# Performance work log

Measured on AMD Instinct MI355X. Metric: run time of the kernel, lower is better.

## Reference

```python
import jax, jax.numpy as jnp
import numpy as np

B = 2048
REAL_NL = 500
NL = 504            # ceil(500/8)*8
NZ = 50
NC = 21
GH = 512            # gru hidden
LRF = 336           # low_res_features
CHS = [336, 168, 84, 42]  # deconv channel ladder
EPS = 1e-5


def setup_inputs() -> dict:
    key = jax.random.key(0)
    ks = iter(jax.random.split(key, 40))
    d = {}
    d["X"] = jax.random.normal(next(ks), (B, REAL_NL, NC), dtype=jnp.float32)
    d["z"] = jax.random.normal(next(ks), (B, NZ), dtype=jnp.float32)
    d["is_training"] = 0
    # Upsampler dense: Linear(NZ -> NL//8 * LRF)
    d["dense_W"] = jax.random.normal(next(ks), (NL // 8 * LRF, NZ), dtype=jnp.float32) * 0.05
    d["dense_b"] = jnp.zeros((NL // 8 * LRF,), dtype=jnp.float32)
    for i in range(3):
        cin, cout = CHS[i], CHS[i + 1]
        d[f"dc{i}_W"] = jax.random.normal(next(ks), (cin, cout, 2), dtype=jnp.float32) * 0.05
        d[f"bn{i}_g"] = jnp.ones((cout,), dtype=jnp.float32)
        d[f"bn{i}_b"] = jnp.zeros((cout,), dtype=jnp.float32)
        d[f"bn{i}_m"] = jax.random.normal(next(ks), (cout,), dtype=jnp.float32) * 0.1
        d[f"bn{i}_v"] = jax.random.uniform(next(ks), (cout,), dtype=jnp.float32, minval=0.5, maxval=1.5)
        d[f"prelu{i}"] = jnp.full((1,), 0.25, dtype=jnp.float32)
    # project_x: Conv1d(NC->NC, k=1) == linear
    d["w_px"] = jax.random.normal(next(ks), (NC, NC), dtype=jnp.float32) * 0.05
    d["b_px"] = jnp.zeros((NC,), dtype=jnp.float32)
    # GRU (1 layer): input = 42 + NC = 63
    gin = CHS[3] + NC
    d["w_ih"] = jax.random.normal(next(ks), (3 * GH, gin), dtype=jnp.float32) * 0.05
    d["w_hh"] = jax.random.normal(next(ks), (3 * GH, GH), dtype=jnp.float32) * 0.05
    d["b_ih"] = jnp.zeros((3 * GH,), dtype=jnp.float32)
    d["b_hh"] = jnp.zeros((3 * GH,), dtype=jnp.float32)
    # output_x: Conv1d(GH->NC, k=1)
    d["w_out"] = jax.random.normal(next(ks), (NC, GH), dtype=jnp.float32) * 0.05
    d["b_out"] = jnp.zeros((NC,), dtype=jnp.float32)
    return d


def _upsample(z, dense_W, dense_b, dcs, bns, alphas):
    b = z.shape[0]
    h = (z @ dense_W.T + dense_b).reshape(b, LRF, NL // 8)  # [B, 336, 63]
    for i in range(3):
        W = dcs[i]  # [cin, cout, 2]
        t = h.shape[-1]
        # ConvTranspose1d k=2 s=2: out[..., 2t+k] = sum_c in[...,c,t] * W[c,:,k]
        h = jnp.einsum('bct,cok->botk', h, W).reshape(b, W.shape[1], 2 * t)
        g, bb, m, v = bns[i]
        h = (h - m[:, None]) * (g[:, None] / jnp.sqrt(v[:, None] + EPS)) + bb[:, None]
        a = alphas[i]
        h = jnp.where(h >= 0, h, a[0] * h)
    return h  # [B, 42, NL]


def reference(X, z, is_training,
              dense_W, dense_b,
              dc0_W, bn0_g, bn0_b, bn0_m, bn0_v, prelu0,
              dc1_W, bn1_g, bn1_b, bn1_m, bn1_v, prelu1,
              dc2_W, bn2_g, bn2_b, bn2_m, bn2_v, prelu2,
              w_px, b_px, w_ih, w_hh, b_ih, b_hh, w_out, b_out):
    h = _upsample(z, dense_W, dense_b,
                  [dc0_W, dc1_W, dc2_W],
                  [(bn0_g, bn0_b, bn0_m, bn0_v), (bn1_g, bn1_b, bn1_m, bn1_v), (bn2_g, bn2_b, bn2_m, bn2_v)],
                  [prelu0, prelu1, prelu2])
    b = z.shape[0]
    hseq = jnp.transpose(h, (2, 0, 1))  # [NL, B, 42]

    def step(carry, h_t):
        gru_h, x1h = carry                       # [B,GH], [B,NC]
        px = x1h @ w_px.T + b_px                 # project_x (1x1 conv)
        x_in = jnp.concatenate([h_t, px], axis=-1)  # [B, 63]
        gi = x_in @ w_ih.T + b_ih
        gh = gru_h @ w_hh.T + b_hh
        ir, iz, inn = jnp.split(gi, 3, axis=-1)
        hr, hz, hn = jnp.split(gh, 3, axis=-1)
        r = jax.nn.sigmoid(ir + hr)
        zt = jax.nn.sigmoid(iz + hz)
        n = jnp.tanh(inn + r * hn)
        h_new = (1.0 - zt) * n + zt * gru_h
        logit = h_new @ w_out.T + b_out          # [B, NC]
        x1h_new = jax.nn.one_hot(jnp.argmax(logit, axis=-1), NC, dtype=logit.dtype)
        return (h_new, x1h_new), logit

    init = (jnp.zeros((b, GH), dtype=z.dtype), jnp.zeros((b, NC), dtype=z.dtype))
    _, logits = jax.lax.scan(step, init, hseq)   # [NL, B, NC]
    out = jnp.transpose(logits, (1, 0, 2))[:, :REAL_NL, :]
    return out
```

## Files before the change

### kernel.cpp

```cpp
#include <hip/hip_runtime.h>
#include <math.h>

#define NLFULL 504
#define REAL_NL 500
#define BATCH 2048
#define NZ 50
#define NC 21
#define GHID 512
#define EPSB 1e-5f
#define LO_SCALE 2048.0f
#define INV_LO (1.0f / 2048.0f)

typedef __attribute__((ext_vector_type(4))) float f32x4;
typedef __attribute__((ext_vector_type(8))) _Float16 half8;

__device__ __forceinline__ void split2(float x, _Float16& hi, _Float16& lo) {
    hi = (_Float16)x;
    lo = (_Float16)((x - (float)hi) * LO_SCALE);
}

__global__ __launch_bounds__(512) void upsample_kernel(
    const float* __restrict__ z, const float* __restrict__ dW, const float* __restrict__ db,
    const float* __restrict__ W0, const float* __restrict__ g0, const float* __restrict__ bb0,
    const float* __restrict__ m0, const float* __restrict__ v0, const float* __restrict__ al0,
    const float* __restrict__ W1, const float* __restrict__ g1, const float* __restrict__ bb1,
    const float* __restrict__ m1, const float* __restrict__ v1, const float* __restrict__ al1,
    const float* __restrict__ W2, const float* __restrict__ g2, const float* __restrict__ bb2,
    const float* __restrict__ m2, const float* __restrict__ v2, const float* __restrict__ al2,
    float* __restrict__ hseq)
{
    __shared__ float bufA[5712];
    __shared__ float bufB[5544];
    __shared__ float zl[52];

    const int b   = blockIdx.x;
    const int ta  = blockIdx.y * 16;
    const int nt0 = min(16, 63 - ta);
    const int tid = threadIdx.x;

    if (tid < NZ) zl[tid] = z[b * NZ + tid];
    __syncthreads();

    for (int i = tid; i < 336 * nt0; i += 512) {
        int c = i % 336, tt = i / 336;
        int row = c * 63 + ta + tt;
        const float* wr = dW + (size_t)row * NZ;
        float s = db[row];
        #pragma unroll
        for (int n = 0; n < NZ; ++n) s += zl[n] * wr[n];
        bufA[c * 17 + tt] = s;
    }
    __syncthreads();

    const float a0 = al0[0], a1 = al1[0], a2 = al2[0];

    for (int i = tid; i < 168 * 2 * nt0; i += 512) {
        int o = i % 168, tt1 = i / 168;
        int tt = tt1 >> 1, k = tt1 & 1;
        const float* wp = W0 + o * 2 + k;
        float s = 0.f;
        for (int c = 0; c < 336; ++c) s += bufA[c * 17 + tt] * wp[c * 336];
        float sc = g0[o] / sqrtf(v0[o] + EPSB);
        s = (s - m0[o]) * sc + bb0[o];
        s = (s >= 0.f) ? s : a0 * s;
        bufB[o * 33 + tt1] = s;
    }
    __syncthreads();

    for (int i = tid; i < 84 * 4 * nt0; i += 512) {
        int o = i % 84, tt2 = i / 84;
        int tt1 = tt2 >> 1, k = tt2 & 1;
// ... 27 lines not shown
{
    int i = blockIdx.x * 256 + threadIdx.x;
    if (i >= 22 * 1536) return;
    int e = i / 1536, jg = i % 1536;
    const float* wih = w_ih + jg * 63 + 42;
    float s = b_ih[jg];
    #pragma unroll
    for (int jp = 0; jp < NC; ++jp) {
        float px = b_px[jp] + (e < NC ? w_px[jp * NC + e] : 0.f);
        s += px * wih[jp];
    }
    table[i] = s;
}

__global__ void pack_whh_kernel(const float* __restrict__ w_hh,
                                _Float16* __restrict__ pH, _Float16* __restrict__ pL)
{
    int i = blockIdx.x * 256 + threadIdx.x;
    if (i >= 3 * 32 * 16 * 512) return;
    int e = i & 7, l = (i >> 3) & 63, kf = (i >> 9) & 15, nf = (i >> 13) & 31, g = i >> 18;
    int n = nf * 16 + (l & 15);
    int k = kf * 32 + ((l >> 4) << 3) + e;
    float v = w_hh[(size_t)(g * GHID + n) * GHID + k];
    _Float16 hi, lo; split2(v, hi, lo);
    pH[i] = hi; pL[i] = lo;
}

__global__ void pack_wih_kernel(const float* __restrict__ w_ih,
                                _Float16* __restrict__ pH, _Float16* __restrict__ pL)
{
    int i = blockIdx.x * 256 + threadIdx.x;
    if (i >= 3 * 32 * 2 * 512) return;
    int e = i & 7, l = (i >> 3) & 63, kf = (i >> 9) & 1, nf = (i >> 10) & 31, g = i >> 15;
    int n = nf * 16 + (l & 15);
    int k = kf * 32 + ((l >> 4) << 3) + e;
    float v = (k < 42) ? w_ih[(size_t)(g * GHID + n) * 63 + k] : 0.f;
    _Float16 hi, lo; split2(v, hi, lo);
    pH[i] = hi; pL[i] = lo;
}

__global__ void pack_wout_kernel(const float* __restrict__ w_out,
                                 _Float16* __restrict__ pH, _Float16* __restrict__ pL)
{
    int i = blockIdx.x * 256 + threadIdx.x;
    if (i >= 2 * 16 * 512) return;
    int e = i & 7, l = (i >> 3) & 63, kf = (i >> 9) & 15, nf = i >> 13;
    int n = nf * 16 + (l & 15);
    int k = kf * 32 + ((l >> 4) << 3) + e;
    float v = (n < NC) ? w_out[(size_t)n * GHID + k] : 0.f;
    _Float16 hi, lo; split2(v, hi, lo);
    pH[i] = hi; pL[i] = lo;
}

__global__ void init_kernel(_Float16* __restrict__ hH, _Float16* __restrict__ hL)
{
    int i = blockIdx.x * 256 + threadIdx.x;
    if (i < BATCH * GHID) { hH[i] = (_Float16)0.f; hL[i] = (_Float16)0.f; }
}

#define MFMA3(mainA, crossA, aH_, aL_, bH_, bL_)                                   \
    mainA  = __builtin_amdgcn_mfma_f32_16x16x32_f16(aH_, bH_, mainA, 0, 0, 0);     \
    crossA = __builtin_amdgcn_mfma_f32_16x16x32_f16(aH_, bL_, crossA, 0, 0, 0);    \
    crossA = __builtin_amdgcn_mfma_f32_16x16x32_f16(aL_, bH_, crossA, 0, 0, 0);

__global__ __launch_bounds__(512, 2) void gru_step(
    const _Float16* __restrict__ hpH, const _Float16* __restrict__ hpL,
    const float* __restrict__ ht,
    const float* __restrict__ table,
    const _Float16* __restrict__ whhH, const _Float16* __restrict__ whhL,
    const _Float16* __restrict__ wihH, const _Float16* __restrict__ wihL,
    const float* __restrict__ b_hh,
    const _Float16* __restrict__ woH, const _Float16* __restrict__ woL,
    const float* __restrict__ b_out,
    float* __restrict__ out, int t,
    _Float16* __restrict__ hnH, _Float16* __restrict__ hnL)
{
    __shared__ float lg[128][33];
    __shared__ int   idx_lds[128];

    const int tid  = threadIdx.x;
    const int l    = tid & 63;
    const int wv   = tid >> 6;
    const int m0   = blockIdx.y * 128;
    const int lrow = l & 15;
    const int lk   = (l >> 4) << 3;

    if (t > 0) {
        const size_t ar = (size_t)(m0 + wv * 16 + lrow) * GHID + lk;
        f32x4 accM[2], accX[2];
        accM[0] = (f32x4)0.f; accM[1] = (f32x4)0.f;
        accX[0] = (f32x4)0.f; accX[1] = (f32x4)0.f;
        for (int kf = 0; kf < 16; ++kf) {
            half8 aH = *(const half8*)(hpH + ar + kf * 32);
            half8 aL = *(const half8*)(hpL + ar + kf * 32);
            #pragma unroll
            for (int nf = 0; nf < 2; ++nf) {
                size_t bo = ((size_t)(nf * 16 + kf) << 9) + (l << 3);
                half8 bH = *(const half8*)(woH + bo);
                half8 bL = *(const half8*)(woL + bo);
                MFMA3(accM[nf], accX[nf], aH, aL, bH, bL);
            }
        }
        #pragma unroll
        for (int nf = 0; nf < 2; ++nf) {
            int col = nf * 16 + lrow;
            float bias = (col < NC) ? b_out[col] : 0.f;
            #pragma unroll
            for (int r = 0; r < 4; ++r) {
                int row = wv * 16 + ((l >> 4) << 2) + r;
                lg[row][col] = accM[nf][r] + accX[nf][r] * INV_LO + bias;
            }
        }
    }
    __syncthreads();
    if (tid < 128) {
        if (t > 0) {
            float best = lg[tid][0]; int bi = 0;
            #pragma unroll
            for (int c = 1; c < NC; ++c) {
                float v = lg[tid][c];
                if (v > best) { best = v; bi = c; }
            }
            idx_lds[tid] = bi;
            if (blockIdx.x == 0) {
                float* op = out + (size_t)(m0 + tid) * (REAL_NL * NC) + (size_t)(t - 1) * NC;
                #pragma unroll
                for (int c = 0; c < NC; ++c) op[c] = lg[tid][c];
            }
        } else {
            idx_lds[tid] = NC;
        }
    }
    __syncthreads();

    if (t >= REAL_NL) return;

    const int wM = wv >> 1, wN = wv & 1;
    const int mw = m0 + wM * 32;
    const int nf = blockIdx.x * 2 + wN;

    f32x4 aM[4][2], aX[4][2];
    #pragma unroll
    for (int s = 0; s < 4; ++s)
        #pragma unroll
        for (int mi = 0; mi < 2; ++mi) { aM[s][mi] = (f32x4)0.f; aX[s][mi] = (f32x4)0.f; }

    const size_t arow0 = (size_t)(mw + lrow) * GHID + lk;
    const size_t arow1 = arow0 + 16 * GHID;

    for (int kf = 0; kf < 16; ++kf) {
        half8 aHf[2], aLf[2];
        aHf[0] = *(const half8*)(hpH + arow0 + kf * 32);
        aLf[0] = *(const half8*)(hpL + arow0 + kf * 32);
        aHf[1] = *(const half8*)(hpH + arow1 + kf * 32);
        aLf[1] = *(const half8*)(hpL + arow1 + kf * 32);
        #pragma unroll
        for (int g = 0; g < 3; ++g) {
            size_t bo = ((size_t)((g * 32 + nf) * 16 + kf) << 9) + (l << 3);
            half8 bH = *(const half8*)(whhH + bo);
            half8 bL = *(const half8*)(whhL + bo);
            const int s = (g == 2) ? 3 : g;
            #pragma unroll
            for (int mi = 0; mi < 2; ++mi) {
                MFMA3(aM[s][mi], aX[s][mi], aHf[mi], aLf[mi], bH, bL);
            }
        }
    }

    #pragma unroll
    for (int kf = 0; kf < 2; ++kf) {
        half8 aHf[2], aLf[2];
        #pragma unroll
        for (int mi = 0; mi < 2; ++mi) {
            const float* rp = ht + (size_t)(mw + mi * 16 + lrow) * 42;
            #pragma unroll
            for (int e = 0; e < 8; ++e) {
                int k = kf * 32 + lk + e;
                float f = (k < 42) ? rp[k] : 0.f;
                _Float16 hi, lo; split2(f, hi, lo);
                aHf[mi][e] = hi; aLf[mi][e] = lo;
            }
        }
        #pragma unroll
        for (int g = 0; g < 3; ++g) {
            size_t bo = ((size_t)((g * 32 + nf) * 2 + kf) << 9) + (l << 3);
            half8 bH = *(const half8*)(wihH + bo);
            half8 bL = *(const half8*)(wihL + bo);
            const int s = (g == 2) ? 2 : g;
            #pragma unroll
            for (int mi = 0; mi < 2; ++mi) {
                MFMA3(aM[s][mi], aX[s][mi], aHf[mi], aLf[mi], bH, bL);
            }
        }
    }

    const int c = nf * 16 + lrow;
    const float bhr = b_hh[c], bhz = b_hh[GHID + c], bhn = b_hh[2 * GHID + c];
    #pragma unroll
    for (int mi = 0; mi < 2; ++mi) {
        #pragma unroll
        for (int r = 0; r < 4; ++r) {
            int lm = wM * 32 + mi * 16 + ((l >> 4) << 2) + r;
            int m = m0 + lm;
            const float* tb = table + idx_lds[lm] * 1536;
            float rv  = aM[0][mi][r] + aX[0][mi][r] * INV_LO + bhr + tb[c];
            float zv  = aM[1][mi][r] + aX[1][mi][r] * INV_LO + bhz + tb[GHID + c];
            float inp = aM[2][mi][r] + aX[2][mi][r] * INV_LO + tb[2 * GHID + c];
            float hnp = aM[3][mi][r] + aX[3][mi][r] * INV_LO + bhn;
            float rg = 1.f / (1.f + expf(-rv));
            float zg = 1.f / (1.f + expf(-zv));
            float ng = tanhf(inp + rg * hnp);
            size_t off = (size_t)m * GHID + c;
            float hpv = (float)hpH[off] + (float)hpL[off] * INV_LO;
            float hnv = (1.f - zg) * ng + zg * hpv;
            _Float16 hi, lo; split2(hnv, hi, lo);
            hnH[off] = hi; hnL[off] = lo;
        }
    }
}

extern "C" void kernel_launch(void* const* d_in, const int* in_sizes, int n_in,
                              void* d_out, int out_size, void* d_ws, size_t ws_size,
                              hipStream_t stream)
{
    const float* z    = (const float*)d_in[1];
    const float* dW   = (const float*)d_in[3];
    const float* db   = (const float*)d_in[4];
    const float* W0   = (const float*)d_in[5];
    const float* g0   = (const float*)d_in[6];
    const float* bb0  = (const float*)d_in[7];
    const float* m0   = (const float*)d_in[8];
    const float* v0   = (const float*)d_in[9];
    const float* al0  = (const float*)d_in[10];
    const float* W1   = (const float*)d_in[11];
    const float* g1   = (const float*)d_in[12];
    const float* bb1  = (const float*)d_in[13];
    const float* m1   = (const float*)d_in[14];
    const float* v1   = (const float*)d_in[15];
    const float* al1  = (const float*)d_in[16];
    const float* W2   = (const float*)d_in[17];
    const float* g2   = (const float*)d_in[18];
    const float* bb2  = (const float*)d_in[19];
    const float* m2   = (const float*)d_in[20];
    const float* v2   = (const float*)d_in[21];
    const float* al2  = (const float*)d_in[22];
    const float* w_px = (const float*)d_in[23];
    const float* b_px = (const float*)d_in[24];
    const float* w_ih = (const float*)d_in[25];
    const float* w_hh = (const float*)d_in[26];
    const float* b_ih = (const float*)d_in[27];
    const float* b_hh = (const float*)d_in[28];
    const float* w_out= (const float*)d_in[29];
    const float* b_out= (const float*)d_in[30];
    float* out = (float*)d_out;

    float* ws = (float*)d_ws;
    float* hseq = ws;
    _Float16* hAH = (_Float16*)(hseq + (size_t)NLFULL * BATCH * 42);
    _Float16* hAL = hAH + (size_t)BATCH * GHID;
    _Float16* hBH = hAL + (size_t)BATCH * GHID;
    _Float16* hBL = hBH + (size_t)BATCH * GHID;
    _Float16* whhH = hBL + (size_t)BATCH * GHID;
    _Float16* whhL = whhH + 3 * 32 * 16 * 512;
    _Float16* wihH = whhL + 3 * 32 * 16 * 512;
    _Float16* wihL = wihH + 3 * 32 * 2 * 512;
    _Float16* woH  = wihL + 3 * 32 * 2 * 512;
    _Float16* woL  = woH + 2 * 16 * 512;
    float* table = (float*)(woL + 2 * 16 * 512);

    upsample_kernel<<<dim3(BATCH, 4), 512, 0, stream>>>(
        z, dW, db,
        W0, g0, bb0, m0, v0, al0,
        W1, g1, bb1, m1, v1, al1,
        W2, g2, bb2, m2, v2, al2,
        hseq);

    table_kernel<<<(22 * 1536 + 255) / 256, 256, 0, stream>>>(w_px, b_px, w_ih, b_ih, table);
    pack_whh_kernel<<<(3 * 32 * 16 * 512 + 255) / 256, 256, 0, stream>>>(w_hh, whhH, whhL);
    pack_wih_kernel<<<(3 * 32 * 2 * 512 + 255) / 256, 256, 0, stream>>>(w_ih, wihH, wihL);
    pack_wout_kernel<<<(2 * 16 * 512 + 255) / 256, 256, 0, stream>>>(w_out, woH, woL);
    init_kernel<<<(BATCH * GHID + 255) / 256, 256, 0, stream>>>(hAH, hAL);

    for (int t = 0; t <= REAL_NL; ++t) {
        const _Float16* pH = (t & 1) ? hBH : hAH;
        const _Float16* pL = (t & 1) ? hBL : hAL;
        _Float16* nH = (t & 1) ? hAH : hBH;
        _Float16* nL = (t & 1) ? hAL : hBL;
        gru_step<<<dim3(16, 16), 512, 0, stream>>>(
            pH, pL, hseq + (size_t)t * BATCH * 42, table,
            whhH, whhL, wihH, wihL, b_hh,
            woH, woL, b_out, out, t, nH, nL);
    }
}
```

Baseline: 34.50 ms.

## Replace per-timestep GRU launches with persistent cooperative kernel and grid barrier

Replaces 501 separate gru_step launches with one persistent cooperative kernel of 256 blocks. The blocks synchronize each timestep through an atomic counter barrier in global memory. The hidden state is stored as interleaved hi/lo fp16 pairs packed into one 32-bit word and read and written with agent-scope relaxed atomics. The tiling also changes to 64-row by 128-column blocks, and the output projection is fused into the same pass over h as the recurrent GEMM. This removes launch overhead and per-step kernel boundaries. The costs are spin-barrier latency, possible visibility or ordering problems from relaxed atomics, and a deadlock risk if the fallback launch does not make all blocks co-resident.

```diff
diff --git a/kernel.cpp b/kernel.cpp
--- a/kernel.cpp
+++ b/kernel.cpp
@@ -13,10 +13,45 @@
 
 typedef __attribute__((ext_vector_type(4))) float f32x4;
 typedef __attribute__((ext_vector_type(8))) _Float16 half8;
+typedef __attribute__((ext_vector_type(4))) unsigned uint4v;
 
 __device__ __forceinline__ void split2(float x, _Float16& hi, _Float16& lo) {
     hi = (_Float16)x;
     lo = (_Float16)((x - (float)hi) * LO_SCALE);
+}
+__device__ __forceinline__ unsigned packh(float x) {
+    _Float16 hi, lo; split2(x, hi, lo);
+    return (unsigned)__builtin_bit_cast(unsigned short, hi)
+         | ((unsigned)__builtin_bit_cast(unsigned short, lo) << 16);
+}
+__device__ __forceinline__ float unpackh(unsigned w) {
+    _Float16 hi = __builtin_bit_cast(_Float16, (unsigned short)(w & 0xFFFFu));
+    _Float16 lo = __builtin_bit_cast(_Float16, (unsigned short)(w >> 16));
+    return (float)hi + (float)lo * INV_LO;
+}
+
+__device__ __forceinline__ void load_hfrag(const unsigned* H, size_t eoff,
+                                           half8& aH, half8& aL) {
+    unsigned long long* p = (unsigned long long*)(H + eoff);
+    unsigned long long d0 = __hip_atomic_load(p + 0, __ATOMIC_RELAXED, __HIP_MEMORY_SCOPE_AGENT);
+    unsigned long long d1 = __hip_atomic_load(p + 1, __ATOMIC_RELAXED, __HIP_MEMORY_SCOPE_AGENT);
+    unsigned long long d2 = __hip_atomic_load(p + 2, __ATOMIC_RELAXED, __HIP_MEMORY_SCOPE_AGENT);
+    unsigned long long d3 = __hip_atomic_load(p + 3, __ATOMIC_RELAXED, __HIP_MEMORY_SCOPE_AGENT);
+    unsigned w0 = (unsigned)d0, w1 = (unsigned)(d0 >> 32);
+    unsigned w2 = (unsigned)d1, w3 = (unsigned)(d1 >> 32);
+    unsigned w4 = (unsigned)d2, w5 = (unsigned)(d2 >> 32);
+    unsigned w6 = (unsigned)d3, w7 = (unsigned)(d3 >> 32);
+    uint4v hw, lw;
+    hw.x = (w0 & 0xFFFFu) | (w1 << 16);
+    hw.y = (w2 & 0xFFFFu) | (w3 << 16);
+    hw.z = (w4 & 0xFFFFu) | (w5 << 16);
+    hw.w = (w6 & 0xFFFFu) | (w7 << 16);
+    lw.x = (w0 >> 16) | (w1 & 0xFFFF0000u);
+    lw.y = (w2 >> 16) | (w3 & 0xFFFF0000u);
+    lw.z = (w4 >> 16) | (w5 & 0xFFFF0000u);
+    lw.w = (w6 >> 16) | (w7 & 0xFFFF0000u);
+    aH = __builtin_bit_cast(half8, hw);
+    aL = __builtin_bit_cast(half8, lw);
 }
 
 __global__ __launch_bounds__(512) void upsample_kernel(
@@ -150,10 +185,11 @@
     pH[i] = hi; pL[i] = lo;
 }
 
-__global__ void init_kernel(_Float16* __restrict__ hH, _Float16* __restrict__ hL)
+__global__ void init_kernel(unsigned* __restrict__ hA, int* __restrict__ bar)
 {
     int i = blockIdx.x * 256 + threadIdx.x;
-    if (i < BATCH * GHID) { hH[i] = (_Float16)0.f; hL[i] = (_Float16)0.f; }
+    if (i < BATCH * GHID) hA[i] = 0u;
+    if (i < 64) bar[i] = 0;
 }
 
 #define MFMA3(mainA, crossA, aH_, aL_, bH_, bL_)                                   \
@@ -161,158 +197,163 @@
     crossA = __builtin_amdgcn_mfma_f32_16x16x32_f16(aH_, bL_, crossA, 0, 0, 0);    \
     crossA = __builtin_amdgcn_mfma_f32_16x16x32_f16(aL_, bH_, crossA, 0, 0, 0);
 
-__global__ __launch_bounds__(512, 2) void gru_step(
-    const _Float16* __restrict__ hpH, const _Float16* __restrict__ hpL,
-    const float* __restrict__ ht,
-    const float* __restrict__ table,
-    const _Float16* __restrict__ whhH, const _Float16* __restrict__ whhL,
-    const _Float16* __restrict__ wihH, const _Float16* __restrict__ wihL,
-    const float* __restrict__ b_hh,
-    const _Float16* __restrict__ woH, const _Float16* __restrict__ woL,
-    const float* __restrict__ b_out,
-    float* __restrict__ out, int t,
-    _Float16* __restrict__ hnH, _Float16* __restrict__ hnL)
-{
-    __shared__ float lg[128][33];
-    __shared__ int   idx_lds[128];
-
-    const int tid  = threadIdx.x;
-    const int l    = tid & 63;
-    const int wv   = tid >> 6;
-    const int m0   = blockIdx.y * 128;
-    const int lrow = l & 15;
-    const int lk   = (l >> 4) << 3;
-
-    if (t > 0) {
-        const size_t ar = (size_t)(m0 + wv * 16 + lrow) * GHID + lk;
-        f32x4 accM[2], accX[2];
-        accM[0] = (f32x4)0.f; accM[1] = (f32x4)0.f;
-        accX[0] = (f32x4)0.f; accX[1] = (f32x4)0.f;
+struct GruP {
+    unsigned *hA, *hB;
+    const float* hseq;
+    const float* table;
+    const _Float16 *whhH, *whhL, *wihH, *wihL, *woH, *woL;
+    const float *b_hh, *b_out;
+    float* out;
+    int* bar;
+};
+
+__global__ __launch_bounds__(512, 1) void gru_persistent(GruP p)
+{
+    __shared__ float lgbuf[64][33];
+    __shared__ int   idx_l[64];
+
+    const int bid = blockIdx.x;
+    const int nb  = bid & 7;
+    const int mb  = bid >> 3;
+    const int m0  = mb * 64;
+    const int tid = threadIdx.x;
+    const int l   = tid & 63, wv = tid >> 6;
+    const int mw  = wv >> 1, nw = wv & 1;
+    const int lrow = l & 15, lk = (l >> 4) << 3;
+
+    const int rowg = m0 + mw * 16 + lrow;
+    const size_t abase = (size_t)rowg * GHID;
+    const int nf0 = nb * 4 + nw * 2;
+    int epoch = 0;
+
+    for (int i = 1; i <= REAL_NL + 1; ++i) {
+        __syncthreads();
+        ++epoch;
+        if (tid == 0) {
+            __hip_atomic_fetch_add(p.bar, 1, __ATOMIC_RELEASE, __HIP_MEMORY_SCOPE_AGENT);
+            while (__hip_atomic_load(p.bar, __ATOMIC_RELAXED, __HIP_MEMORY_SCOPE_AGENT)
+                   < epoch * 256)
+                __builtin_amdgcn_s_sleep(1);
+        }
+        __syncthreads();
+
+        const unsigned* Hp = (i & 1) ? p.hA : p.hB;
+        unsigned*       Hn = (i & 1) ? p.hB : p.hA;
+        const float*    ht = p.hseq + (size_t)(i - 1) * (BATCH * 42);
+        const bool    do_g = (i <= REAL_NL);
+
+        f32x4 gM[4][2], gX[4][2];
+        f32x4 lM = (f32x4)0.f, lX = (f32x4)0.f;
+        #pragma unroll
+        for (int s = 0; s < 4; ++s)
+            #pragma unroll
+            for (int cc = 0; cc < 2; ++cc) { gM[s][cc] = (f32x4)0.f; gX[s][cc] = (f32x4)0.f; }
+
         for (int kf = 0; kf < 16; ++kf) {
-            half8 aH = *(const half8*)(hpH + ar + kf * 32);
-            half8 aL = *(const half8*)(hpL + ar + kf * 32);
+            half8 aH, aL;
+            load_hfrag(Hp, abase + kf * 32 + lk, aH, aL);
+            {
+                size_t bo = ((size_t)(nw * 16 + kf) << 9) + (l << 3);
+                half8 bH = *(const half8*)(p.woH + bo);
+                half8 bL = *(const half8*)(p.woL + bo);
+                MFMA3(lM, lX, aH, aL, bH, bL);
+            }
+            if (do_g) {
+                #pragma unroll
+                for (int g = 0; g < 3; ++g) {
+                    #pragma unroll
+                    for (int cc = 0; cc < 2; ++cc) {
+                        size_t bo = ((size_t)((g * 32 + nf0 + cc) * 16 + kf) << 9) + (l << 3);
+                        half8 bH = *(const half8*)(p.whhH + bo);
+                        half8 bL = *(const half8*)(p.whhL + bo);
+                        const int s = (g == 2) ? 3 : g;
+                        MFMA3(gM[s][cc], gX[s][cc], aH, aL, bH, bL);
+                    }
+                }
+            }
+        }
+
+        if (do_g) {
             #pragma unroll
-            for (int nf = 0; nf < 2; ++nf) {
-                size_t bo = ((size_t)(nf * 16 + kf) << 9) + (l << 3);
-                half8 bH = *(const half8*)(woH + bo);
-                half8 bL = *(const half8*)(woL + bo);
-                MFMA3(accM[nf], accX[nf], aH, aL, bH, bL);
-            }
-        }
-        #pragma unroll
-        for (int nf = 0; nf < 2; ++nf) {
-            int col = nf * 16 + lrow;
-            float bias = (col < NC) ? b_out[col] : 0.f;
+            for (int kf = 0; kf < 2; ++kf) {
+                half8 aH, aL;
+                const float* rp = ht + (size_t)rowg * 42;
+                #pragma unroll
+                for (int e = 0; e < 8; ++e) {
+                    int k = kf * 32 + lk + e;
+                    float f = (k < 42) ? rp[k] : 0.f;
+                    _Float16 hi, lo; split2(f, hi, lo);
+                    aH[e] = hi; aL[e] = lo;
+                }
+                #pragma unroll
+                for (int g = 0; g < 3; ++g) {
+                    #pragma unroll
+                    for (int cc = 0; cc < 2; ++cc) {
+                        size_t bo = ((size_t)((g * 32 + nf0 + cc) * 2 + kf) << 9) + (l << 3);
+                        half8 bH = *(const half8*)(p.wihH + bo);
+                        half8 bL = *(const half8*)(p.wihL + bo);
+                        const int s = (g == 2) ? 2 : g;
+                        MFMA3(gM[s][cc], gX[s][cc], aH, aL, bH, bL);
+                    }
+                }
+            }
+        }
+
+        {
+            int col = nw * 16 + lrow;
+            float bias = (col < NC) ? p.b_out[col] : 0.f;
             #pragma unroll
             for (int r = 0; r < 4; ++r) {
-                int row = wv * 16 + ((l >> 4) << 2) + r;
-                lg[row][col] = accM[nf][r] + accX[nf][r] * INV_LO + bias;
-            }
-        }
-    }
-    __syncthreads();
-    if (tid < 128) {
-        if (t > 0) {
-            float best = lg[tid][0]; int bi = 0;
+                int row = mw * 16 + ((l >> 4) << 2) + r;
+                lgbuf[row][col] = lM[r] + lX[r] * INV_LO + bias;
+            }
+        }
+        __syncthreads();
+        if (tid < 64) {
+            int bi = NC;
+            if (i > 1) {
+                float best = lgbuf[tid][0]; bi = 0;
+                #pragma unroll
+                for (int c = 1; c < NC; ++c) {
+                    float v = lgbuf[tid][c];
+                    if (v > best) { best = v; bi = c; }
+                }
+                if (nb == 0) {
+                    float* op = p.out + (size_t)(m0 + tid) * (REAL_NL * NC)
+                                      + (size_t)(i - 2) * NC;
+                    #pragma unroll
+                    for (int c = 0; c < NC; ++c) op[c] = lgbuf[tid][c];
+                }
+            }
+            idx_l[tid] = bi;
+        }
+        __syncthreads();
+
+        if (do_g) {
             #pragma unroll
-            for (int c = 1; c < NC; ++c) {
-                float v = lg[tid][c];
-                if (v > best) { best = v; bi = c; }
-            }
-            idx_lds[tid] = bi;
-            if (blockIdx.x == 0) {
-                float* op = out + (size_t)(m0 + tid) * (REAL_NL * NC) + (size_t)(t - 1) * NC;
+            for (int cc = 0; cc < 2; ++cc) {
+                int c = (nf0 + cc) * 16 + lrow;
+                float bhr = p.b_hh[c], bhz = p.b_hh[GHID + c], bhn = p.b_hh[2 * GHID + c];
                 #pragma unroll
-                for (int c = 0; c < NC; ++c) op[c] = lg[tid][c];
-            }
-        } else {
-            idx_lds[tid] = NC;
-        }
-    }
-    __syncthreads();
-
-    if (t >= REAL_NL) return;
-
-    const int wM = wv >> 1, wN = wv & 1;
-    const int mw = m0 + wM * 32;
-    const int nf = blockIdx.x * 2 + wN;
-
-    f32x4 aM[4][2], aX[4][2];
-    #pragma unroll
-    for (int s = 0; s < 4; ++s)
-        #pragma unroll
-        for (int mi = 0; mi < 2; ++mi) { aM[s][mi] = (f32x4)0.f; aX[s][mi] = (f32x4)0.f; }
-
-    const size_t arow0 = (size_t)(mw + lrow) * GHID + lk;
-    const size_t arow1 = arow0 + 16 * GHID;
-
-    for (int kf = 0; kf < 16; ++kf) {
-        half8 aHf[2], aLf[2];
-        aHf[0] = *(const half8*)(hpH + arow0 + kf * 32);
-        aLf[0] = *(const half8*)(hpL + arow0 + kf * 32);
-        aHf[1] = *(const half8*)(hpH + arow1 + kf * 32);
-        aLf[1] = *(const half8*)(hpL + arow1 + kf * 32);
-        #pragma unroll
-        for (int g = 0; g < 3; ++g) {
-            size_t bo = ((size_t)((g * 32 + nf) * 16 + kf) << 9) + (l << 3);
-            half8 bH = *(const half8*)(whhH + bo);
-            half8 bL = *(const half8*)(whhL + bo);
-            const int s = (g == 2) ? 3 : g;
-            #pragma unroll
-            for (int mi = 0; mi < 2; ++mi) {
-                MFMA3(aM[s][mi], aX[s][mi], aHf[mi], aLf[mi], bH, bL);
-            }
-        }
-    }
-
-    #pragma unroll
-    for (int kf = 0; kf < 2; ++kf) {
-        half8 aHf[2], aLf[2];
-        #pragma unroll
-        for (int mi = 0; mi < 2; ++mi) {
-            const float* rp = ht + (size_t)(mw + mi * 16 + lrow) * 42;
-            #pragma unroll
-            for (int e = 0; e < 8; ++e) {
-                int k = kf * 32 + lk + e;
-                float f = (k < 42) ? rp[k] : 0.f;
-                _Float16 hi, lo; split2(f, hi, lo);
-                aHf[mi][e] = hi; aLf[mi][e] = lo;
-            }
-        }
-        #pragma unroll
-        for (int g = 0; g < 3; ++g) {
-            size_t bo = ((size_t)((g * 32 + nf) * 2 + kf) << 9) + (l << 3);
-            half8 bH = *(const half8*)(wihH + bo);
-            half8 bL = *(const half8*)(wihL + bo);
-            const int s = (g == 2) ? 2 : g;
-            #pragma unroll
-            for (int mi = 0; mi < 2; ++mi) {
-                MFMA3(aM[s][mi], aX[s][mi], aHf[mi], aLf[mi], bH, bL);
-            }
-        }
-    }
-
-    const int c = nf * 16 + lrow;
-    const float bhr = b_hh[c], bhz = b_hh[GHID + c], bhn = b_hh[2 * GHID + c];
-    #pragma unroll
-    for (int mi = 0; mi < 2; ++mi) {
-        #pragma unroll
-        for (int r = 0; r < 4; ++r) {
-            int lm = wM * 32 + mi * 16 + ((l >> 4) << 2) + r;
-            int m = m0 + lm;
-            const float* tb = table + idx_lds[lm] * 1536;
-            float rv  = aM[0][mi][r] + aX[0][mi][r] * INV_LO + bhr + tb[c];
-            float zv  = aM[1][mi][r] + aX[1][mi][r] * INV_LO + bhz + tb[GHID + c];
-            float inp = aM[2][mi][r] + aX[2][mi][r] * INV_LO + tb[2 * GHID + c];
-            float hnp = aM[3][mi][r] + aX[3][mi][r] * INV_LO + bhn;
-            float rg = 1.f / (1.f + expf(-rv));
-            float zg = 1.f / (1.f + expf(-zv));
-            float ng = tanhf(inp + rg * hnp);
-            size_t off = (size_t)m * GHID + c;
-            float hpv = (float)hpH[off] + (float)hpL[off] * INV_LO;
-            float hnv = (1.f - zg) * ng + zg * hpv;
-            _Float16 hi, lo; split2(hnv, hi, lo);
-            hnH[off] = hi; hnL[off] = lo;
+                for (int r = 0; r < 4; ++r) {
+                    int lm = mw * 16 + ((l >> 4) << 2) + r;
+                    int m = m0 + lm;
+                    const float* tb = p.table + idx_l[lm] * 1536;
+                    float rv  = gM[0][cc][r] + gX[0][cc][r] * INV_LO + bhr + tb[c];
+                    float zv  = gM[1][cc][r] + gX[1][cc][r] * INV_LO + bhz + tb[GHID + c];
+                    float inp = gM[2][cc][r] + gX[2][cc][r] * INV_LO + tb[2 * GHID + c];
+                    float hnp = gM[3][cc][r] + gX[3][cc][r] * INV_LO + bhn;
+                    float rg = 1.f / (1.f + expf(-rv));
+                    float zg = 1.f / (1.f + expf(-zv));
+                    float ng = tanhf(inp + rg * hnp);
+                    size_t off = (size_t)m * GHID + c;
+                    unsigned wprev = __hip_atomic_load((unsigned*)Hp + off,
+                                                       __ATOMIC_RELAXED, __HIP_MEMORY_SCOPE_AGENT);
+                    float hnv = (1.f - zg) * ng + zg * unpackh(wprev);
+                    __hip_atomic_store(Hn + off, packh(hnv),
+                                       __ATOMIC_RELAXED, __HIP_MEMORY_SCOPE_AGENT);
+                }
+            }
         }
     }
 }
@@ -354,17 +395,16 @@
 
     float* ws = (float*)d_ws;
     float* hseq = ws;
-    _Float16* hAH = (_Float16*)(hseq + (size_t)NLFULL * BATCH * 42);
-    _Float16* hAL = hAH + (size_t)BATCH * GHID;
-    _Float16* hBH = hAL + (size_t)BATCH * GHID;
-    _Float16* hBL = hBH + (size_t)BATCH * GHID;
-    _Float16* whhH = hBL + (size_t)BATCH * GHID;
+    unsigned* hA = (unsigned*)(hseq + (size_t)NLFULL * BATCH * 42);
+    unsigned* hB = hA + (size_t)BATCH * GHID;
+    _Float16* whhH = (_Float16*)(hB + (size_t)BATCH * GHID);
     _Float16* whhL = whhH + 3 * 32 * 16 * 512;
     _Float16* wihH = whhL + 3 * 32 * 16 * 512;
     _Float16* wihL = wihH + 3 * 32 * 2 * 512;
     _Float16* woH  = wihL + 3 * 32 * 2 * 512;
     _Float16* woL  = woH + 2 * 16 * 512;
     float* table = (float*)(woL + 2 * 16 * 512);
+    int*   bar   = (int*)(table + 22 * 1536);
 
     upsample_kernel<<<dim3(BATCH, 4), 512, 0, stream>>>(
         z, dW, db,
@@ -377,16 +417,20 @@
     pack_whh_kernel<<<(3 * 32 * 16 * 512 + 255) / 256, 256, 0, stream>>>(w_hh, whhH, whhL);
     pack_wih_kernel<<<(3 * 32 * 2 * 512 + 255) / 256, 256, 0, stream>>>(w_ih, wihH, wihL);
     pack_wout_kernel<<<(2 * 16 * 512 + 255) / 256, 256, 0, stream>>>(w_out, woH, woL);
-    init_kernel<<<(BATCH * GHID + 255) / 256, 256, 0, stream>>>(hAH, hAL);
-
-    for (int t = 0; t <= REAL_NL; ++t) {
-        const _Float16* pH = (t & 1) ? hBH : hAH;
-        const _Float16* pL = (t & 1) ? hBL : hAL;
-        _Float16* nH = (t & 1) ? hAH : hBH;
-        _Float16* nL = (t & 1) ? hAL : hBL;
-        gru_step<<<dim3(16, 16), 512, 0, stream>>>(
-            pH, pL, hseq + (size_t)t * BATCH * 42, table,
-            whhH, whhL, wihH, wihL, b_hh,
-            woH, woL, b_out, out, t, nH, nL);
-    }
-}
+    init_kernel<<<(BATCH * GHID + 255) / 256, 256, 0, stream>>>(hA, bar);
+
+    GruP p;
+    p.hA = hA; p.hB = hB;
+    p.hseq = hseq; p.table = table;
+    p.whhH = whhH; p.whhL = whhL; p.wihH = wihH; p.wihL = wihL;
+    p.woH = woH; p.woL = woL;
+    p.b_hh = b_hh; p.b_out = b_out;
+    p.out = out; p.bar = bar;
+
+    void* args[] = { &p };
+    hipError_t e = hipLaunchCooperativeKernel((void*)gru_persistent,
+                                              dim3(256), dim3(512), args, 0, stream);
+    if (e != hipSuccess) {
+        gru_persistent<<<256, 512, 0, stream>>>(p);
+    }
+}
```

Result: slower. 87.45 ms (+153.5%).

## Fuse all GRU timesteps into one persistent kernel with LDS-resident hidden state

Applied to the files above, without the earlier changes.

Replaces the 501 per-timestep gru_step launches with a single persistent kernel. Each of 256 blocks owns 8 batch rows and keeps their hidden state (hi/lo fp16 split) double-buffered in swizzled LDS across all timesteps. The output projection, argmax and the prefetch of the next step's input are folded into the same loop, which removes launch overhead and global-memory round trips of the hidden state. In exchange, every block now streams the full packed W_hh from cache on every step, and the 16-row MFMA tiles hold only 8 real rows, so half of the matrix work is padding.

```diff
diff --git a/kernel.cpp b/kernel.cpp
--- a/kernel.cpp
+++ b/kernel.cpp
@@ -150,170 +150,164 @@
     pH[i] = hi; pL[i] = lo;
 }
 
-__global__ void init_kernel(_Float16* __restrict__ hH, _Float16* __restrict__ hL)
-{
-    int i = blockIdx.x * 256 + threadIdx.x;
-    if (i < BATCH * GHID) { hH[i] = (_Float16)0.f; hL[i] = (_Float16)0.f; }
-}
-
 #define MFMA3(mainA, crossA, aH_, aL_, bH_, bL_)                                   \
     mainA  = __builtin_amdgcn_mfma_f32_16x16x32_f16(aH_, bH_, mainA, 0, 0, 0);     \
     crossA = __builtin_amdgcn_mfma_f32_16x16x32_f16(aH_, bL_, crossA, 0, 0, 0);    \
     crossA = __builtin_amdgcn_mfma_f32_16x16x32_f16(aL_, bH_, crossA, 0, 0, 0);
 
-__global__ __launch_bounds__(512, 2) void gru_step(
-    const _Float16* __restrict__ hpH, const _Float16* __restrict__ hpL,
-    const float* __restrict__ ht,
+__device__ __forceinline__ int hswz(int row, int k) {
+    return row * 512 + (k ^ ((row & 7) << 3));
+}
+__device__ __forceinline__ int tswz(int row, int k) {
+    return row * 64 + (k ^ ((row & 7) << 3));
+}
+
+__global__ __launch_bounds__(512, 1) void gru_rows(
+    const float* __restrict__ hseq,
     const float* __restrict__ table,
     const _Float16* __restrict__ whhH, const _Float16* __restrict__ whhL,
     const _Float16* __restrict__ wihH, const _Float16* __restrict__ wihL,
-    const float* __restrict__ b_hh,
-    const _Float16* __restrict__ woH, const _Float16* __restrict__ woL,
-    const float* __restrict__ b_out,
-    float* __restrict__ out, int t,
-    _Float16* __restrict__ hnH, _Float16* __restrict__ hnL)
-{
-    __shared__ float lg[128][33];
-    __shared__ int   idx_lds[128];
+    const _Float16* __restrict__ woH,  const _Float16* __restrict__ woL,
+    const float* __restrict__ b_hh, const float* __restrict__ b_out,
+    float* __restrict__ out)
+{
+    __shared__ _Float16 hHi[2][16 * 512];
+    __shared__ _Float16 hLo[2][16 * 512];
+    __shared__ _Float16 tHi[2][16 * 64];
+    __shared__ _Float16 tLo[2][16 * 64];
+    __shared__ float    lgbuf[8][32];
+    __shared__ int      idx_l[8];
 
     const int tid  = threadIdx.x;
-    const int l    = tid & 63;
-    const int wv   = tid >> 6;
-    const int m0   = blockIdx.y * 128;
-    const int lrow = l & 15;
-    const int lk   = (l >> 4) << 3;
-
-    if (t > 0) {
-        const size_t ar = (size_t)(m0 + wv * 16 + lrow) * GHID + lk;
-        f32x4 accM[2], accX[2];
-        accM[0] = (f32x4)0.f; accM[1] = (f32x4)0.f;
-        accX[0] = (f32x4)0.f; accX[1] = (f32x4)0.f;
-        for (int kf = 0; kf < 16; ++kf) {
-            half8 aH = *(const half8*)(hpH + ar + kf * 32);
-            half8 aL = *(const half8*)(hpL + ar + kf * 32);
+    const int l    = tid & 63, wv = tid >> 6;
+    const int lrow = l & 15, lk = (l >> 4) << 3;
+    const int row0 = blockIdx.x * 8;
+
+    for (int i = tid; i < 16 * 512; i += 512) {
+        hHi[0][i] = (_Float16)0.f; hHi[1][i] = (_Float16)0.f;
+        hLo[0][i] = (_Float16)0.f; hLo[1][i] = (_Float16)0.f;
+    }
+    for (int i = tid; i < 16 * 64; i += 512) {
+        tHi[0][i] = (_Float16)0.f; tHi[1][i] = (_Float16)0.f;
+        tLo[0][i] = (_Float16)0.f; tLo[1][i] = (_Float16)0.f;
+    }
+    if (tid < 8) idx_l[tid] = NC;
+    __syncthreads();
+    if (tid < 336) {
+        int r = tid / 42, k = tid % 42;
+        float f = hseq[(size_t)(row0 + r) * 42 + k];
+        _Float16 hi, lo; split2(f, hi, lo);
+        int o = tswz(r, k);
+        tHi[0][o] = hi; tLo[0][o] = lo;
+    }
+    __syncthreads();
+
+    for (int t = 0; t < REAL_NL; ++t) {
+        const int pp = t & 1, pn = pp ^ 1;
+
+        #pragma unroll
+        for (int jj = 0; jj < 4; ++jj) {
+            const int nf = wv + jj * 8;
+            f32x4 aM[4], aX[4];
             #pragma unroll
-            for (int nf = 0; nf < 2; ++nf) {
-                size_t bo = ((size_t)(nf * 16 + kf) << 9) + (l << 3);
+            for (int s = 0; s < 4; ++s) { aM[s] = (f32x4)0.f; aX[s] = (f32x4)0.f; }
+
+            for (int kf = 0; kf < 16; ++kf) {
+                int ao = hswz(lrow, kf * 32 + lk);
+                half8 aH = *(const half8*)(&hHi[pp][ao]);
+                half8 aL = *(const half8*)(&hLo[pp][ao]);
+                #pragma unroll
+                for (int g = 0; g < 3; ++g) {
+                    size_t bo = ((size_t)((g * 32 + nf) * 16 + kf) << 9) + (l << 3);
+                    half8 bH = *(const half8*)(whhH + bo);
+                    half8 bL = *(const half8*)(whhL + bo);
+                    const int s = (g == 2) ? 3 : g;
+                    MFMA3(aM[s], aX[s], aH, aL, bH, bL);
+                }
+            }
+            #pragma unroll
+            for (int kf = 0; kf < 2; ++kf) {
+                int ao = tswz(lrow, kf * 32 + lk);
+                half8 aH = *(const half8*)(&tHi[pp][ao]);
+                half8 aL = *(const half8*)(&tLo[pp][ao]);
+                #pragma unroll
+                for (int g = 0; g < 3; ++g) {
+                    size_t bo = ((size_t)((g * 32 + nf) * 2 + kf) << 9) + (l << 3);
+                    half8 bH = *(const half8*)(wihH + bo);
+                    half8 bL = *(const half8*)(wihL + bo);
+                    const int s = (g == 2) ? 2 : g;
+                    MFMA3(aM[s], aX[s], aH, aL, bH, bL);
+                }
+            }
+            if (l < 32) {
+                const int c = nf * 16 + lrow;
+                const float bhr = b_hh[c], bhz = b_hh[GHID + c], bhn = b_hh[2 * GHID + c];
+                #pragma unroll
+                for (int r = 0; r < 4; ++r) {
+                    int row = ((l >> 4) << 2) + r;
+                    const float* tb = table + idx_l[row] * 1536;
+                    float rv  = aM[0][r] + aX[0][r] * INV_LO + bhr + tb[c];
+                    float zv  = aM[1][r] + aX[1][r] * INV_LO + bhz + tb[GHID + c];
+                    float inp = aM[2][r] + aX[2][r] * INV_LO + tb[2 * GHID + c];
+                    float hnp = aM[3][r] + aX[3][r] * INV_LO + bhn;
+                    float rg = 1.f / (1.f + expf(-rv));
+                    float zg = 1.f / (1.f + expf(-zv));
+                    float ng = tanhf(inp + rg * hnp);
+                    int ho = hswz(row, c);
+                    float hpv = (float)hHi[pp][ho] + (float)hLo[pp][ho] * INV_LO;
+                    float hnv = (1.f - zg) * ng + zg * hpv;
+                    _Float16 hi, lo; split2(hnv, hi, lo);
+                    hHi[pn][ho] = hi; hLo[pn][ho] = lo;
+                }
+            }
+        }
+        __syncthreads();
+
+        if (wv < 2) {
+            f32x4 lM = (f32x4)0.f, lX = (f32x4)0.f;
+            for (int kf = 0; kf < 16; ++kf) {
+                int ao = hswz(lrow, kf * 32 + lk);
+                half8 aH = *(const half8*)(&hHi[pn][ao]);
+                half8 aL = *(const half8*)(&hLo[pn][ao]);
+                size_t bo = ((size_t)(wv * 16 + kf) << 9) + (l << 3);
                 half8 bH = *(const half8*)(woH + bo);
                 half8 bL = *(const half8*)(woL + bo);
-                MFMA3(accM[nf], accX[nf], aH, aL, bH, bL);
+                MFMA3(lM, lX, aH, aL, bH, bL);
+            }
+            if (l < 32) {
+                int col = wv * 16 + lrow;
+                float bias = (col < NC) ? b_out[col] : 0.f;
+                #pragma unroll
+                for (int r = 0; r < 4; ++r) {
+                    int row = ((l >> 4) << 2) + r;
+                    lgbuf[row][col] = lM[r] + lX[r] * INV_LO + bias;
+                }
+            }
+        } else {
+            int s = tid - 128;
+            if (s < 336) {
+                int r = s / 42, k = s % 42;
+                float f = hseq[(size_t)(t + 1) * (BATCH * 42) + (size_t)(row0 + r) * 42 + k];
+                _Float16 hi, lo; split2(f, hi, lo);
+                int o = tswz(r, k);
+                tHi[pn][o] = hi; tLo[pn][o] = lo;
             }
         }
-        #pragma unroll
-        for (int nf = 0; nf < 2; ++nf) {
-            int col = nf * 16 + lrow;
-            float bias = (col < NC) ? b_out[col] : 0.f;
-            #pragma unroll
-            for (int r = 0; r < 4; ++r) {
-                int row = wv * 16 + ((l >> 4) << 2) + r;
-                lg[row][col] = accM[nf][r] + accX[nf][r] * INV_LO + bias;
-            }
-        }
-    }
-    __syncthreads();
-    if (tid < 128) {
-        if (t > 0) {
-            float best = lg[tid][0]; int bi = 0;
+        __syncthreads();
+
+        if (tid < 8) {
+            float best = lgbuf[tid][0]; int bi = 0;
             #pragma unroll
             for (int c = 1; c < NC; ++c) {
-                float v = lg[tid][c];
+                float v = lgbuf[tid][c];
                 if (v > best) { best = v; bi = c; }
             }
-            idx_lds[tid] = bi;
-            if (blockIdx.x == 0) {
-                float* op = out + (size_t)(m0 + tid) * (REAL_NL * NC) + (size_t)(t - 1) * NC;
-                #pragma unroll
-                for (int c = 0; c < NC; ++c) op[c] = lg[tid][c];
-            }
-        } else {
-            idx_lds[tid] = NC;
+            idx_l[tid] = bi;
+            float* op = out + (size_t)(row0 + tid) * (REAL_NL * NC) + (size_t)t * NC;
+            #pragma unroll
+            for (int c = 0; c < NC; ++c) op[c] = lgbuf[tid][c];
         }
-    }
-    __syncthreads();
-
-    if (t >= REAL_NL) return;
-
-    const int wM = wv >> 1, wN = wv & 1;
-    const int mw = m0 + wM * 32;
-    const int nf = blockIdx.x * 2 + wN;
-
-    f32x4 aM[4][2], aX[4][2];
-    #pragma unroll
-    for (int s = 0; s < 4; ++s)
-        #pragma unroll
-        for (int mi = 0; mi < 2; ++mi) { aM[s][mi] = (f32x4)0.f; aX[s][mi] = (f32x4)0.f; }
-
-    const size_t arow0 = (size_t)(mw + lrow) * GHID + lk;
-    const size_t arow1 = arow0 + 16 * GHID;
-
-    for (int kf = 0; kf < 16; ++kf) {
-        half8 aHf[2], aLf[2];
-        aHf[0] = *(const half8*)(hpH + arow0 + kf * 32);
-        aLf[0] = *(const half8*)(hpL + arow0 + kf * 32);
-        aHf[1] = *(const half8*)(hpH + arow1 + kf * 32);
-        aLf[1] = *(const half8*)(hpL + arow1 + kf * 32);
-        #pragma unroll
-        for (int g = 0; g < 3; ++g) {
-            size_t bo = ((size_t)((g * 32 + nf) * 16 + kf) << 9) + (l << 3);
-            half8 bH = *(const half8*)(whhH + bo);
-            half8 bL = *(const half8*)(whhL + bo);
-            const int s = (g == 2) ? 3 : g;
-            #pragma unroll
-            for (int mi = 0; mi < 2; ++mi) {
-                MFMA3(aM[s][mi], aX[s][mi], aHf[mi], aLf[mi], bH, bL);
-            }
-        }
-    }
-
-    #pragma unroll
-    for (int kf = 0; kf < 2; ++kf) {
-        half8 aHf[2], aLf[2];
-        #pragma unroll
-        for (int mi = 0; mi < 2; ++mi) {
-            const float* rp = ht + (size_t)(mw + mi * 16 + lrow) * 42;
-            #pragma unroll
-            for (int e = 0; e < 8; ++e) {
-                int k = kf * 32 + lk + e;
-                float f = (k < 42) ? rp[k] : 0.f;
-                _Float16 hi, lo; split2(f, hi, lo);
-                aHf[mi][e] = hi; aLf[mi][e] = lo;
-            }
-        }
-        #pragma unroll
-        for (int g = 0; g < 3; ++g) {
-            size_t bo = ((size_t)((g * 32 + nf) * 2 + kf) << 9) + (l << 3);
-            half8 bH = *(const half8*)(wihH + bo);
-            half8 bL = *(const half8*)(wihL + bo);
-            const int s = (g == 2) ? 2 : g;
-            #pragma unroll
-            for (int mi = 0; mi < 2; ++mi) {
-                MFMA3(aM[s][mi], aX[s][mi], aHf[mi], aLf[mi], bH, bL);
-            }
-        }
-    }
-
-    const int c = nf * 16 + lrow;
-    const float bhr = b_hh[c], bhz = b_hh[GHID + c], bhn = b_hh[2 * GHID + c];
-    #pragma unroll
-    for (int mi = 0; mi < 2; ++mi) {
-        #pragma unroll
-        for (int r = 0; r < 4; ++r) {
-            int lm = wM * 32 + mi * 16 + ((l >> 4) << 2) + r;
-            int m = m0 + lm;
-            const float* tb = table + idx_lds[lm] * 1536;
-            float rv  = aM[0][mi][r] + aX[0][mi][r] * INV_LO + bhr + tb[c];
-            float zv  = aM[1][mi][r] + aX[1][mi][r] * INV_LO + bhz + tb[GHID + c];
-            float inp = aM[2][mi][r] + aX[2][mi][r] * INV_LO + tb[2 * GHID + c];
-            float hnp = aM[3][mi][r] + aX[3][mi][r] * INV_LO + bhn;
-            float rg = 1.f / (1.f + expf(-rv));
-            float zg = 1.f / (1.f + expf(-zv));
-            float ng = tanhf(inp + rg * hnp);
-            size_t off = (size_t)m * GHID + c;
-            float hpv = (float)hpH[off] + (float)hpL[off] * INV_LO;
-            float hnv = (1.f - zg) * ng + zg * hpv;
-            _Float16 hi, lo; split2(hnv, hi, lo);
-            hnH[off] = hi; hnL[off] = lo;
-        }
+        __syncthreads();
     }
 }
 
@@ -354,11 +348,7 @@
 
     float* ws = (float*)d_ws;
     float* hseq = ws;
-    _Float16* hAH = (_Float16*)(hseq + (size_t)NLFULL * BATCH * 42);
-    _Float16* hAL = hAH + (size_t)BATCH * GHID;
-    _Float16* hBH = hAL + (size_t)BATCH * GHID;
-    _Float16* hBL = hBH + (size_t)BATCH * GHID;
-    _Float16* whhH = hBL + (size_t)BATCH * GHID;
+    _Float16* whhH = (_Float16*)(hseq + (size_t)NLFULL * BATCH * 42);
     _Float16* whhL = whhH + 3 * 32 * 16 * 512;
     _Float16* wihH = whhL + 3 * 32 * 16 * 512;
     _Float16* wihL = wihH + 3 * 32 * 2 * 512;
@@ -377,16 +367,7 @@
     pack_whh_kernel<<<(3 * 32 * 16 * 512 + 255) / 256, 256, 0, stream>>>(w_hh, whhH, whhL);
     pack_wih_kernel<<<(3 * 32 * 2 * 512 + 255) / 256, 256, 0, stream>>>(w_ih, wihH, wihL);
     pack_wout_kernel<<<(2 * 16 * 512 + 255) / 256, 256, 0, stream>>>(w_out, woH, woL);
-    init_kernel<<<(BATCH * GHID + 255) / 256, 256, 0, stream>>>(hAH, hAL);
-
-    for (int t = 0; t <= REAL_NL; ++t) {
-        const _Float16* pH = (t & 1) ? hBH : hAH;
-        const _Float16* pL = (t & 1) ? hBL : hAL;
-        _Float16* nH = (t & 1) ? hAH : hBH;
-        _Float16* nL = (t & 1) ? hAL : hBL;
-        gru_step<<<dim3(16, 16), 512, 0, stream>>>(
-            pH, pL, hseq + (size_t)t * BATCH * 42, table,
-            whhH, whhL, wihH, wihL, b_hh,
-            woH, woL, b_out, out, t, nH, nL);
-    }
-}
+
+    gru_rows<<<256, 512, 0, stream>>>(
+        hseq, table, whhH, whhL, wihH, wihL, woH, woL, b_hh, b_out, out);
+}
```

Measured after the change: 114.9 ms. 233% more time.

## Retile GRU step to 64-row by 64-column blocks with per-wave column pairs

Applied to the files above, without the earlier changes.

Changes the gru_step grid from 16x16 blocks of 128 batch rows by 32 hidden columns to 8x32 blocks of 64 rows by 64 columns. Each wave now handles one 16-row A fragment against two 16-column B fragments, instead of two A fragments against one B fragment. The recomputed logits/argmax prologue now covers 64 rows per block using all 8 waves, which halves redundant output-projection work per block. In exchange, weight fragment loads per wave double and the launch-bounds occupancy hint of 2 blocks per CU is removed.

```diff
diff --git a/kernel.cpp b/kernel.cpp
--- a/kernel.cpp
+++ b/kernel.cpp
@@ -161,7 +161,7 @@
     crossA = __builtin_amdgcn_mfma_f32_16x16x32_f16(aH_, bL_, crossA, 0, 0, 0);    \
     crossA = __builtin_amdgcn_mfma_f32_16x16x32_f16(aL_, bH_, crossA, 0, 0, 0);
 
-__global__ __launch_bounds__(512, 2) void gru_step(
+__global__ __launch_bounds__(512) void gru_step(
     const _Float16* __restrict__ hpH, const _Float16* __restrict__ hpL,
     const float* __restrict__ ht,
     const float* __restrict__ table,
@@ -173,138 +173,124 @@
     float* __restrict__ out, int t,
     _Float16* __restrict__ hnH, _Float16* __restrict__ hnL)
 {
-    __shared__ float lg[128][33];
-    __shared__ int   idx_lds[128];
+    __shared__ float lg[64][33];
+    __shared__ int   idx_lds[64];
 
     const int tid  = threadIdx.x;
     const int l    = tid & 63;
     const int wv   = tid >> 6;
-    const int m0   = blockIdx.y * 128;
+    const int m0   = blockIdx.y * 64;
     const int lrow = l & 15;
     const int lk   = (l >> 4) << 3;
+    const int af   = wv & 3;
+
+    const size_t arow = (size_t)(m0 + af * 16 + lrow) * GHID + lk;
 
     if (t > 0) {
-        const size_t ar = (size_t)(m0 + wv * 16 + lrow) * GHID + lk;
-        f32x4 accM[2], accX[2];
-        accM[0] = (f32x4)0.f; accM[1] = (f32x4)0.f;
-        accX[0] = (f32x4)0.f; accX[1] = (f32x4)0.f;
+        const int nfl = wv >> 2;
+        f32x4 accM = (f32x4)0.f, accX = (f32x4)0.f;
         for (int kf = 0; kf < 16; ++kf) {
-            half8 aH = *(const half8*)(hpH + ar + kf * 32);
-            half8 aL = *(const half8*)(hpL + ar + kf * 32);
-            #pragma unroll
-            for (int nf = 0; nf < 2; ++nf) {
-                size_t bo = ((size_t)(nf * 16 + kf) << 9) + (l << 3);
-                half8 bH = *(const half8*)(woH + bo);
-                half8 bL = *(const half8*)(woL + bo);
-                MFMA3(accM[nf], accX[nf], aH, aL, bH, bL);
-            }
-        }
-        #pragma unroll
-        for (int nf = 0; nf < 2; ++nf) {
-            int col = nf * 16 + lrow;
-            float bias = (col < NC) ? b_out[col] : 0.f;
-            #pragma unroll
-            for (int r = 0; r < 4; ++r) {
-                int row = wv * 16 + ((l >> 4) << 2) + r;
-                lg[row][col] = accM[nf][r] + accX[nf][r] * INV_LO + bias;
-            }
-        }
-    }
-    __syncthreads();
-    if (tid < 128) {
+            half8 aH = *(const half8*)(hpH + arow + kf * 32);
+            half8 aL = *(const half8*)(hpL + arow + kf * 32);
+            size_t bo = ((size_t)(nfl * 16 + kf) << 9) + (l << 3);
+            half8 bH = *(const half8*)(woH + bo);
+            half8 bL = *(const half8*)(woL + bo);
+            MFMA3(accM, accX, aH, aL, bH, bL);
+        }
+        int col = nfl * 16 + lrow;
+        float bias = (col < NC) ? b_out[col] : 0.f;
+        #pragma unroll
+        for (int r = 0; r < 4; ++r) {
+            int row = af * 16 + ((l >> 4) << 2) + r;
+            lg[row][col] = accM[r] + accX[r] * INV_LO + bias;
+        }
+    }
+    __syncthreads();
+    if (tid < 64) {
+        int bi = NC;
         if (t > 0) {
-            float best = lg[tid][0]; int bi = 0;
+            float best = lg[tid][0]; bi = 0;
             #pragma unroll
             for (int c = 1; c < NC; ++c) {
                 float v = lg[tid][c];
                 if (v > best) { best = v; bi = c; }
             }
-            idx_lds[tid] = bi;
             if (blockIdx.x == 0) {
-                float* op = out + (size_t)(m0 + tid) * (REAL_NL * NC) + (size_t)(t - 1) * NC;
+                float* op = out + (size_t)(m0 + tid) * (REAL_NL * NC)
+                                + (size_t)(t - 1) * NC;
                 #pragma unroll
                 for (int c = 0; c < NC; ++c) op[c] = lg[tid][c];
             }
-        } else {
-            idx_lds[tid] = NC;
-        }
+        }
+        idx_lds[tid] = bi;
     }
     __syncthreads();
 
     if (t >= REAL_NL) return;
 
-    const int wM = wv >> 1, wN = wv & 1;
-    const int mw = m0 + wM * 32;
-    const int nf = blockIdx.x * 2 + wN;
-
-    f32x4 aM[4][2], aX[4][2];
+    const int nfb = (wv >> 2) * 2;
+    f32x4 gM[4][2], gX[4][2];
     #pragma unroll
     for (int s = 0; s < 4; ++s)
         #pragma unroll
-        for (int mi = 0; mi < 2; ++mi) { aM[s][mi] = (f32x4)0.f; aX[s][mi] = (f32x4)0.f; }
-
-    const size_t arow0 = (size_t)(mw + lrow) * GHID + lk;
-    const size_t arow1 = arow0 + 16 * GHID;
+        for (int cc = 0; cc < 2; ++cc) { gM[s][cc] = (f32x4)0.f; gX[s][cc] = (f32x4)0.f; }
 
     for (int kf = 0; kf < 16; ++kf) {
-        half8 aHf[2], aLf[2];
-        aHf[0] = *(const half8*)(hpH + arow0 + kf * 32);
-        aLf[0] = *(const half8*)(hpL + arow0 + kf * 32);
-        aHf[1] = *(const half8*)(hpH + arow1 + kf * 32);
-        aLf[1] = *(const half8*)(hpL + arow1 + kf * 32);
+        half8 aH = *(const half8*)(hpH + arow + kf * 32);
+        half8 aL = *(const half8*)(hpL + arow + kf * 32);
         #pragma unroll
         for (int g = 0; g < 3; ++g) {
-            size_t bo = ((size_t)((g * 32 + nf) * 16 + kf) << 9) + (l << 3);
-            half8 bH = *(const half8*)(whhH + bo);
-            half8 bL = *(const half8*)(whhL + bo);
-            const int s = (g == 2) ? 3 : g;
             #pragma unroll
-            for (int mi = 0; mi < 2; ++mi) {
-                MFMA3(aM[s][mi], aX[s][mi], aHf[mi], aLf[mi], bH, bL);
+            for (int cc = 0; cc < 2; ++cc) {
+                int nfg = blockIdx.x * 4 + nfb + cc;
+                size_t bo = ((size_t)((g * 32 + nfg) * 16 + kf) << 9) + (l << 3);
+                half8 bH = *(const half8*)(whhH + bo);
+                half8 bL = *(const half8*)(whhL + bo);
+                const int s = (g == 2) ? 3 : g;
+                MFMA3(gM[s][cc], gX[s][cc], aH, aL, bH, bL);
             }
         }
     }
 
     #pragma unroll
     for (int kf = 0; kf < 2; ++kf) {
-        half8 aHf[2], aLf[2];
-        #pragma unroll
-        for (int mi = 0; mi < 2; ++mi) {
-            const float* rp = ht + (size_t)(mw + mi * 16 + lrow) * 42;
+        half8 aH, aL;
+        const float* rp = ht + (size_t)(m0 + af * 16 + lrow) * 42;
+        #pragma unroll
+        for (int e = 0; e < 8; ++e) {
+            int k = kf * 32 + lk + e;
+            float f = (k < 42) ? rp[k] : 0.f;
+            _Float16 hi, lo; split2(f, hi, lo);
+            aH[e] = hi; aL[e] = lo;
+        }
+        #pragma unroll
+        for (int g = 0; g < 3; ++g) {
             #pragma unroll
-            for (int e = 0; e < 8; ++e) {
-                int k = kf * 32 + lk + e;
-                float f = (k < 42) ? rp[k] : 0.f;
-                _Float16 hi, lo; split2(f, hi, lo);
-                aHf[mi][e] = hi; aLf[mi][e] = lo;
+            for (int cc = 0; cc < 2; ++cc) {
+                int nfg = blockIdx.x * 4 + nfb + cc;
+                size_t bo = ((size_t)((g * 32 + nfg) * 2 + kf) << 9) + (l << 3);
+                half8 bH = *(const half8*)(wihH + bo);
+                half8 bL = *(const half8*)(wihL + bo);
+                const int s = (g == 2) ? 2 : g;
+                MFMA3(gM[s][cc], gX[s][cc], aH, aL, bH, bL);
             }
         }
-        #pragma unroll
-        for (int g = 0; g < 3; ++g) {
-            size_t bo = ((size_t)((g * 32 + nf) * 2 + kf) << 9) + (l << 3);
-            half8 bH = *(const half8*)(wihH + bo);
-            half8 bL = *(const half8*)(wihL + bo);
-            const int s = (g == 2) ? 2 : g;
-            #pragma unroll
-            for (int mi = 0; mi < 2; ++mi) {
-                MFMA3(aM[s][mi], aX[s][mi], aHf[mi], aLf[mi], bH, bL);
-            }
-        }
-    }
-
-    const int c = nf * 16 + lrow;
-    const float bhr = b_hh[c], bhz = b_hh[GHID + c], bhn = b_hh[2 * GHID + c];
+    }
+
     #pragma unroll
-    for (int mi = 0; mi < 2; ++mi) {
+    for (int cc = 0; cc < 2; ++cc) {
+        int nfg = blockIdx.x * 4 + nfb + cc;
+        int c = nfg * 16 + lrow;
+        float bhr = b_hh[c], bhz = b_hh[GHID + c], bhn = b_hh[2 * GHID + c];
         #pragma unroll
         for (int r = 0; r < 4; ++r) {
-            int lm = wM * 32 + mi * 16 + ((l >> 4) << 2) + r;
+            int lm = af * 16 + ((l >> 4) << 2) + r;
             int m = m0 + lm;
             const float* tb = table + idx_lds[lm] * 1536;
-            float rv  = aM[0][mi][r] + aX[0][mi][r] * INV_LO + bhr + tb[c];
-            float zv  = aM[1][mi][r] + aX[1][mi][r] * INV_LO + bhz + tb[GHID + c];
-            float inp = aM[2][mi][r] + aX[2][mi][r] * INV_LO + tb[2 * GHID + c];
-            float hnp = aM[3][mi][r] + aX[3][mi][r] * INV_LO + bhn;
+            float rv  = gM[0][cc][r] + gX[0][cc][r] * INV_LO + bhr + tb[c];
+            float zv  = gM[1][cc][r] + gX[1][cc][r] * INV_LO + bhz + tb[GHID + c];
+            float inp = gM[2][cc][r] + gX[2][cc][r] * INV_LO + tb[2 * GHID + c];
+            float hnp = gM[3][cc][r] + gX[3][cc][r] * INV_LO + bhn;
             float rg = 1.f / (1.f + expf(-rv));
             float zg = 1.f / (1.f + expf(-zv));
             float ng = tanhf(inp + rg * hnp);
@@ -384,7 +370,7 @@
         const _Float16* pL = (t & 1) ? hBL : hAL;
         _Float16* nH = (t & 1) ? hAH : hBH;
         _Float16* nL = (t & 1) ? hAL : hBL;
-        gru_step<<<dim3(16, 16), 512, 0, stream>>>(
+        gru_step<<<dim3(8, 32), 512, 0, stream>>>(
             pH, pL, hseq + (size_t)t * BATCH * 42, table,
             whhH, whhL, wihH, wihL, b_hh,
             woH, woL, b_out, out, t, nH, nL);
```

After: 39.55 ms. 14.6% more time.
